# Performance work log

Measured on AMD Instinct MI355X. Metric: run time of the kernel, lower is better.

## Reference

```python
import jax, jax.numpy as jnp
import numpy as np

H = 1024

def setup_inputs() -> dict:
    key = jax.random.key(0)
    k1, k2, k3, k4 = jax.random.split(key, 4)
    hidden = jax.random.normal(k1, (1, 64, H), dtype=jnp.float32)
    encoder_outputs = jax.random.normal(k2, (2048, 64, H), dtype=jnp.float32)
    # nn.Linear(H, H) params: weight [out,in], bias [out]
    W = jax.random.normal(k3, (H, H), dtype=jnp.float32) * (1.0 / np.sqrt(H))
    b = jax.random.normal(k4, (H,), dtype=jnp.float32) * 0.01
    return {"hidden": hidden, "encoder_outputs": encoder_outputs, "W": W, "b": b}

def reference(hidden, encoder_outputs, W, b):
    # method == 'general': energy[l,b] = hidden[0,b] . (W @ enc[l,b] + bias)
    # enc: [L, B, H]; projected: [L, B, H]
    proj = jnp.einsum('lbh,kh->lbk', encoder_outputs, W) + b
    # attn_energies: [B, L]
    attn_energies = jnp.einsum('bh,lbh->bl', hidden[0], proj)
    # faithful to F.softmax(..., dim=0): softmax over the BATCH axis
    attn = jax.nn.softmax(attn_energies, axis=0)
    return attn[:, None, :]  # [B, 1, L]
```

## Files before the change

### kernel.cpp

```cpp
#include <hip/hip_runtime.h>
#include <hip/hip_bf16.h>

#define H 1024
#define B 64
#define KC 8
#define KLEN (H / KC)
#define LT 4

__global__ __launch_bounds__(256) void projA1(
    const float* __restrict__ hidden,
    const float* __restrict__ W,
    float* __restrict__ part)
{
    const int b0 = blockIdx.x * 2;
    const int kc = blockIdx.y;
    const int t  = threadIdx.x;
    const float* h0 = hidden + (size_t)b0 * H + (size_t)kc * KLEN;
    const float* h1 = h0 + H;
    const float4* Wr = (const float4*)(W + (size_t)kc * KLEN * H) + t;

    float4 a0 = {0.f, 0.f, 0.f, 0.f};
    float4 a1 = {0.f, 0.f, 0.f, 0.f};
    #pragma unroll 8
    for (int k = 0; k < KLEN; ++k) {
        const float4 w = Wr[(size_t)k * (H / 4)];
        const float s0 = h0[k];
        const float s1 = h1[k];
        a0.x += s0 * w.x; a0.y += s0 * w.y; a0.z += s0 * w.z; a0.w += s0 * w.w;
        a1.x += s1 * w.x; a1.y += s1 * w.y; a1.z += s1 * w.z; a1.w += s1 * w.w;
    }
    ((float4*)(part + ((size_t)kc * B + b0) * H))[t]     = a0;
    ((float4*)(part + ((size_t)kc * B + b0 + 1) * H))[t] = a1;
}

__global__ __launch_bounds__(256) void projA2(
    const float* __restrict__ part,
    const float* __restrict__ hidden,
    const float* __restrict__ bias,
    float* __restrict__ u,
    float* __restrict__ c)
{
    const int b = blockIdx.x;
    const int t = threadIdx.x;

    float4 a = {0.f, 0.f, 0.f, 0.f};
    #pragma unroll
    for (int kc = 0; kc < KC; ++kc) {
        const float4 p = ((const float4*)(part + ((size_t)kc * B + b) * H))[t];
        a.x += p.x; a.y += p.y; a.z += p.z; a.w += p.w;
    }
    ((float4*)(u + (size_t)b * H))[t] = a;

    float s = 0.f;
    #pragma unroll
    for (int j = 0; j < H / 256; ++j)
        s += hidden[(size_t)b * H + t + j * 256] * bias[t + j * 256];
    __shared__ float red[256];
    red[t] = s;
    __syncthreads();
    for (int st = 128; st > 0; st >>= 1) {
        if (t < st) red[t] += red[t + st];
        __syncthreads();
    }
    if (t == 0) c[b] = red[0];
}

__global__ __launch_bounds__(1024) void energy_softmax_fused(
    const float* __restrict__ enc,
    const float* __restrict__ u,
    const float* __restrict__ c,
    float* __restrict__ out,
    int L)
{
    const int l0   = blockIdx.x * LT;
    const int wave = threadIdx.x >> 6;
    const int lane = threadIdx.x & 63;
    const int b0   = wave * 4;

    __shared__ float e_s[LT][B];

    float4 uv[4][4];
    float  cv[4];
    #pragma unroll
    for (int j = 0; j < 4; ++j) {
        const float4* u4 = (const float4*)(u + (size_t)(b0 + j) * H);
        #pragma unroll
        for (int q = 0; q < 4; ++q) uv[j][q] = u4[lane + q * 64];
        cv[j] = c[b0 + j];
    }

    #pragma unroll 1
    for (int i = 0; i < LT; ++i) {
        const int l = l0 + i;
        #pragma unroll
        for (int j = 0; j < 4; ++j) {
            const int b = b0 + j;
            const float4* e4 = (const float4*)(enc + ((size_t)l * B + b) * H);
            float acc = 0.f;
            #pragma unroll
            for (int q = 0; q < 4; ++q) {
                const float4 v = e4[lane + q * 64];
                acc += v.x * uv[j][q].x + v.y * uv[j][q].y
                     + v.z * uv[j][q].z + v.w * uv[j][q].w;
            }
            for (int off = 32; off > 0; off >>= 1) acc += __shfl_down(acc, off, 64);
            if (lane == 0) e_s[i][b] = acc + cv[j];
        }
    }
    __syncthreads();

    if (wave < LT) {
        const float e = e_s[wave][lane];
        float m = e;
        #pragma unroll
        for (int off = 32; off > 0; off >>= 1) m = fmaxf(m, __shfl_xor(m, off, 64));
        const float ex = __expf(e - m);
        float s = ex;
        #pragma unroll
        for (int off = 32; off > 0; off >>= 1) s += __shfl_xor(s, off, 64);
        e_s[wave][lane] = ex / s;
    }
    __syncthreads();

    if (threadIdx.x < B * LT) {
        const int b  = threadIdx.x >> 2;
        const int li = threadIdx.x & 3;
        out[(size_t)b * L + l0 + li] = e_s[li][b];
    }
}

extern "C" void kernel_launch(void* const* d_in, const int* in_sizes, int n_in,
                              void* d_out, int out_size, void* d_ws, size_t ws_size,
                              hipStream_t stream) {
    const float* hidden = (const float*)d_in[0];
    const float* enc    = (const float*)d_in[1];
    const float* W      = (const float*)d_in[2];
    const float* bias   = (const float*)d_in[3];
    float* out = (float*)d_out;

    const int L = in_sizes[1] / (B * H);

    float* part = (float*)d_ws;
    float* u    = part + (size_t)KC * B * H;
    float* c    = u + (size_t)B * H;

    dim3 gridA1(B / 2, KC);
    projA1<<<gridA1, 256, 0, stream>>>(hidden, W, part);

    projA2<<<B, 256, 0, stream>>>(part, hidden, bias, u, c);

    energy_softmax_fused<<<L / LT, 1024, 0, stream>>>(enc, u, c, out, L);
}
```

Baseline: 116.2 us.

## Restructure energy kernel: smaller blocks, nontemporal enc loads, u from cache

```diff
diff --git a/kernel.cpp b/kernel.cpp
--- a/kernel.cpp
+++ b/kernel.cpp
@@ -5,7 +5,9 @@
 #define B 64
 #define KC 8
 #define KLEN (H / KC)
-#define LT 4
+#define LT 2
+
+typedef float floatx4 __attribute__((ext_vector_type(4)));
 
 __global__ __launch_bounds__(256) void projA1(
     const float* __restrict__ hidden,
@@ -65,7 +67,7 @@
     if (t == 0) c[b] = red[0];
 }
 
-__global__ __launch_bounds__(1024) void energy_softmax_fused(
+__global__ __launch_bounds__(256) void energy_softmax_fused(
     const float* __restrict__ enc,
     const float* __restrict__ u,
     const float* __restrict__ c,
@@ -75,36 +77,28 @@
     const int l0   = blockIdx.x * LT;
     const int wave = threadIdx.x >> 6;
     const int lane = threadIdx.x & 63;
-    const int b0   = wave * 4;
 
     __shared__ float e_s[LT][B];
 
-    float4 uv[4][4];
-    float  cv[4];
     #pragma unroll
-    for (int j = 0; j < 4; ++j) {
-        const float4* u4 = (const float4*)(u + (size_t)(b0 + j) * H);
-        #pragma unroll
-        for (int q = 0; q < 4; ++q) uv[j][q] = u4[lane + q * 64];
-        cv[j] = c[b0 + j];
-    }
-
-    #pragma unroll 1
     for (int i = 0; i < LT; ++i) {
         const int l = l0 + i;
-        #pragma unroll
-        for (int j = 0; j < 4; ++j) {
-            const int b = b0 + j;
-            const float4* e4 = (const float4*)(enc + ((size_t)l * B + b) * H);
+        const float* encl = enc + (size_t)l * B * H;
+        #pragma unroll 4
+        for (int j = 0; j < 16; ++j) {
+            const int b = wave * 16 + j;
+            const floatx4* e4 = (const floatx4*)(encl + (size_t)b * H);
+            const float4*  u4 = (const float4*)(u + (size_t)b * H);
             float acc = 0.f;
             #pragma unroll
             for (int q = 0; q < 4; ++q) {
-                const float4 v = e4[lane + q * 64];
-                acc += v.x * uv[j][q].x + v.y * uv[j][q].y
-                     + v.z * uv[j][q].z + v.w * uv[j][q].w;
+                const floatx4 v  = __builtin_nontemporal_load(e4 + lane + q * 64);
+                const float4  uu = u4[lane + q * 64];
+                acc += v.x * uu.x + v.y * uu.y + v.z * uu.z + v.w * uu.w;
             }
+            #pragma unroll
             for (int off = 32; off > 0; off >>= 1) acc += __shfl_down(acc, off, 64);
-            if (lane == 0) e_s[i][b] = acc + cv[j];
+            if (lane == 0) e_s[i][b] = acc + c[b];
         }
     }
     __syncthreads();
@@ -118,14 +112,7 @@
         float s = ex;
         #pragma unroll
         for (int off = 32; off > 0; off >>= 1) s += __shfl_xor(s, off, 64);
-        e_s[wave][lane] = ex / s;
-    }
-    __syncthreads();
-
-    if (threadIdx.x < B * LT) {
-        const int b  = threadIdx.x >> 2;
-        const int li = threadIdx.x & 3;
-        out[(size_t)b * L + l0 + li] = e_s[li][b];
+        out[(size_t)lane * L + l0 + wave] = ex / s;
     }
 }
 
@@ -149,5 +136,5 @@
 
     projA2<<<B, 256, 0, stream>>>(part, hidden, bias, u, c);
 
-    energy_softmax_fused<<<L / LT, 1024, 0, stream>>>(enc, u, c, out, L);
+    energy_softmax_fused<<<L / LT, 256, 0, stream>>>(enc, u, c, out, L);
 }
```

Measured after the change: 117.0 us. Within noise of the previous version (+0.6%).
